# Kernel tuning notes

Hardware: AMD Instinct MI355X
Metric: run time of the kernel (lower is better)

The kernel has to match this reference:

```python
import jax, jax.numpy as jnp
import numpy as np
import math

B, T, D, H = 4, 2048, 1024, 8
DK = D // H


def _rel_shift(x):
    # x: [B, H, T, P] with P = 2T-1 (Transformer-XL relative shift)
    b, h, q, p = x.shape
    x = jnp.pad(x, ((0, 0), (0, 0), (0, 0), (1, 0)))
    x = x.reshape(b, h, p + 1, q)[:, :, 1:]
    return x.reshape(b, h, q, p)


def setup_inputs() -> dict:
    key = jax.random.key(0)
    ks = jax.random.split(key, 9)
    s = 0.02
    x = jax.random.normal(ks[0], (B, T, D), jnp.float32)
    pos_emb = jax.random.normal(ks[1], (1, 2 * T - 1, D), jnp.float32)
    Wq = jax.random.normal(ks[2], (D, D), jnp.float32) * s
    Wk = jax.random.normal(ks[3], (D, D), jnp.float32) * s
    Wv = jax.random.normal(ks[4], (D, D), jnp.float32) * s
    Wo = jax.random.normal(ks[5], (D, D), jnp.float32) * s
    Wp = jax.random.normal(ks[6], (D, D), jnp.float32) * s
    pos_bias_u = jax.random.normal(ks[7], (H, DK), jnp.float32) * s
    pos_bias_v = jax.random.normal(ks[8], (H, DK), jnp.float32) * s
    return {"x": x, "pos_emb": pos_emb, "Wq": Wq, "Wk": Wk, "Wv": Wv,
            "Wo": Wo, "Wp": Wp, "pos_bias_u": pos_bias_u, "pos_bias_v": pos_bias_v}


def reference(x, pos_emb, Wq, Wk, Wv, Wo, Wp, pos_bias_u, pos_bias_v):
    b, t, d = x.shape
    h, dk = pos_bias_u.shape
    inv_sdk = 1.0 / math.sqrt(dk)
    # projections (torch Linear: y = x @ W.T)
    q = (x @ Wq.T).reshape(b, t, h, dk)          # [B,T,H,DK]
    k = (x @ Wk.T).reshape(b, t, h, dk)          # [B,T,H,DK]
    v = (x @ Wv.T).reshape(b, t, h, dk)          # [B,T,H,DK]
    p = (pos_emb @ Wp.T).reshape(-1, h, dk)      # [P,H,DK], P = 2T-1
    # content and position scores
    matrix_ac = jnp.einsum('bqhd,bkhd->bhqk', q + pos_bias_u, k)   # [B,H,T,T]
    matrix_bd = jnp.einsum('bqhd,phd->bhqp', q + pos_bias_v, p)    # [B,H,T,2T-1]
    matrix_bd = _rel_shift(matrix_bd)[..., :t]                     # [B,H,T,T]
    scores = (matrix_ac + matrix_bd) * inv_sdk
    attn = jax.nn.softmax(scores, axis=-1)
    out = jnp.einsum('bhqk,bkhd->bqhd', attn, v).reshape(b, t, h * dk)
    return out @ Wo.T
```

## Files before the change

### kernel.cpp

```cpp
#include <hip/hip_runtime.h>
#include <cstdint>
#include <math.h>

#define B_   4
#define T_   2048
#define D_   1024
#define H_   8
#define DK_  128
#define P_   4095
#define PS_  4096

typedef unsigned short ushort_t;
typedef __attribute__((ext_vector_type(8))) short short8;
typedef __attribute__((ext_vector_type(4))) float floatx4;

__device__ inline float bf2f(ushort_t s) {
    return __uint_as_float(((unsigned int)s) << 16);
}
__device__ inline ushort_t f2bf(float f) {
    unsigned int u = __float_as_uint(f);
    u += 0x7fffu + ((u >> 16) & 1u);
    return (ushort_t)(u >> 16);
}

__device__ inline floatx4 mfma16(short8 a, short8 b, floatx4 c) {
    return __builtin_amdgcn_mfma_f32_16x16x32_bf16(a, b, c, 0, 0, 0);
}

__device__ inline void gload_lds16(const ushort_t* g, ushort_t* l) {
    __builtin_amdgcn_global_load_lds(
        (const __attribute__((address_space(1))) unsigned int*)g,
        (__attribute__((address_space(3))) unsigned int*)l, 16, 0, 0);
}

__device__ inline float rowmax16(float x) {
    int t;
    t = __builtin_amdgcn_update_dpp(0, __float_as_int(x), 0x128, 0xf, 0xf, true);
    x = fmaxf(x, __int_as_float(t));
    t = __builtin_amdgcn_update_dpp(0, __float_as_int(x), 0x124, 0xf, 0xf, true);
    x = fmaxf(x, __int_as_float(t));
    t = __builtin_amdgcn_update_dpp(0, __float_as_int(x), 0x4E, 0xf, 0xf, true);
    x = fmaxf(x, __int_as_float(t));
    t = __builtin_amdgcn_update_dpp(0, __float_as_int(x), 0xB1, 0xf, 0xf, true);
    x = fmaxf(x, __int_as_float(t));
    return x;
}

__global__ void detect_kernel(const ushort_t* x, int* flag) {
    if (blockIdx.x == 0 && threadIdx.x == 0) {
        int m = 0;
        for (int i = 0; i < 64; ++i) {
            float v = bf2f(x[2 * i]);
            float a = fabsf(v);
            if (!(a == 0.0f || (a > 1e-20f && a < 1e10f))) m = 1;
        }
        flag[0] = m;
    }
}

#define CV_TOT 17826816
template <int MODE>
__global__ __launch_bounds__(256) void convert_kernel(
    const int* __restrict__ flag,
    const void* __restrict__ x, const void* __restrict__ pe,
    const void* __restrict__ wq, const void* __restrict__ wk,
    const void* __restrict__ wv, const void* __restrict__ wo,
    const void* __restrict__ wp, const void* __restrict__ ub,
    const void* __restrict__ vb, ushort_t* __restrict__ dst)
{
    if (flag[0] != MODE) return;
    const size_t i = ((size_t)blockIdx.x * 256 + threadIdx.x) * 4;
    if (i >= CV_TOT) return;
    const void* s; size_t off;
    if (i < 8388608)       { s = x;  off = i; }
    else if (i < 12581888) { s = pe; off = i - 8388608; }
    else if (i < 13630464) { s = wq; off = i - 12581888; }
    else if (i < 14679040) { s = wk; off = i - 13630464; }
    else if (i < 15727616) { s = wv; off = i - 14679040; }
    else if (i < 16776192) { s = wo; off = i - 15727616; }
    else if (i < 17824768) { s = wp; off = i - 16776192; }
    else if (i < 17825792) { s = ub; off = i - 17824768; }
    else                   { s = vb; off = i - 17825792; }
    const size_t d = i + (i >= 12581888 ? 1024 : 0);
    if (MODE == 0) {
        *(uint2*)(dst + d) = *(const uint2*)((const ushort_t*)s + off);
    } else {
        float4 f = *(const float4*)((const float*)s + off);
        uint2 o;
        o.x = (unsigned)f2bf(f.x) | ((unsigned)f2bf(f.y) << 16);
        o.y = (unsigned)f2bf(f.z) | ((unsigned)f2bf(f.w) << 16);
        *(uint2*)(dst + d) = o;
    }
}

__global__ __launch_bounds__(256, 3) void gemm_mfma(
    const int* __restrict__ flag,
    const ushort_t* __restrict__ A, const ushort_t* __restrict__ W,
    void* __restrict__ C, int smode)
{
    if (smode == 3 && flag[0] != 0) return;
    if (smode == 4 && flag[0] != 1) return;
    const int K = 1024, N = 1024;

    __shared__ ushort_t Al[16 * 512];
    __shared__ ushort_t Wl[16 * 512];

    const int tid  = threadIdx.x;
    const int w    = tid >> 6, lane = tid & 63;
    const int r15  = lane & 15, quad = lane >> 4;
    const int wm   = w >> 1, wn = w & 1;
    const int m0   = blockIdx.y * 128, n0 = blockIdx.x * 128;

    floatx4 acc[4][4];
    const floatx4 z4 = {0.f, 0.f, 0.f, 0.f};
#pragma unroll
    for (int mt = 0; mt < 4; ++mt)
#pragma unroll
        for (int nt = 0; nt < 4; ++nt) acc[mt][nt] = z4;

    for (int k0 = 0; k0 < K; k0 += 64) {
#pragma unroll
        for (int ss = 0; ss < 4; ++ss) {
            const int s  = w * 4 + ss;
            const int mg = s >> 1, ks = s & 1;
            const int row = mg * 16 + r15;
            const int col = k0 + ks * 32 + quad * 8;
            gload_lds16(A + (size_t)(m0 + row) * K + col, &Al[s * 512]);
            gload_lds16(W + (size_t)(n0 + row) * K + col, &Wl[s * 512]);
        }
        __syncthreads();

        short8 af[2][4], bf[2][4];
#pragma unroll
        for (int ks = 0; ks < 2; ++ks) {
#pragma unroll
            for (int mt = 0; mt < 4; ++mt)
                af[ks][mt] = *(const short8*)&Al[(((wm * 4 + mt) * 2 + ks) * 64 + lane) * 8];
#pragma unroll
            for (int nt = 0; nt < 4; ++nt)
                bf[ks][nt] = *(const short8*)&Wl[(((wn * 4 + nt) * 2 + ks) * 64 + lane) * 8];
        }
#pragma unroll
        for (int ks = 0; ks < 2; ++ks)
#pragma unroll
            for (int mt = 0; mt < 4; ++mt)
#pragma unroll
                for (int nt = 0; nt < 4; ++nt)
                    acc[mt][nt] = mfma16(af[ks][mt], bf[ks][nt], acc[mt][nt]);
        __syncthreads();
    }

#pragma unroll
    for (int mt = 0; mt < 4; ++mt)
#pragma unroll
        for (int nt = 0; nt < 4; ++nt)
#pragma unroll
            for (int i = 0; i < 4; ++i) {
                const int m = m0 + wm * 64 + mt * 16 + quad * 4 + i;
                const int n = n0 + wn * 64 + nt * 16 + r15;
                const float v = acc[mt][nt][i];
                if (smode == 0) {
                    const int b = m >> 11, t = m & (T_ - 1);
                    const int h = n >> 7, dk = n & (DK_ - 1);
                    ((ushort_t*)C)[(((size_t)(b * H_ + h)) * T_ + t) * DK_ + dk] = f2bf(v);
                } else if (smode == 1) {
                    const int h = n >> 7, dk = n & (DK_ - 1);
                    ((ushort_t*)C)[((size_t)h * PS_ + m) * DK_ + dk] = f2bf(v);
                } else if (smode == 2) {
                    const int b = m >> 11, t = m & (T_ - 1);
                    const int h = n >> 7, dk = n & (DK_ - 1);
                    ((ushort_t*)C)[((size_t)(b * H_ + h) * DK_ + dk) * T_ + t] = f2bf(v);
                } else if (smode == 3) {
                    ((ushort_t*)C)[(size_t)m * N + n] = f2bf(v);
                } else {
                    ((float*)C)[(size_t)m * N + n] = v;
                }
            }
}

__global__ __launch_bounds__(256, 2) void attn_mfma(
    const ushort_t* __restrict__ qg,
    const ushort_t* __restrict__ kgl,
    const ushort_t* __restrict__ vt,
    const ushort_t* __restrict__ pg,
    const ushort_t* __restrict__ ubb,
    const ushort_t* __restrict__ vbb,
    ushort_t* __restrict__ ao)
{
    __shared__ ushort_t K_lds[16 * 512];
    __shared__ ushort_t V_lds[16 * 512];
    __shared__ ushort_t P_lds[32 * 512];
    __shared__ __align__(16) ushort_t pr_lds[4][1024];

    const int tid  = threadIdx.x;
    const int w    = tid >> 6;
    const int lane = tid & 63;
    const int r15  = lane & 15;
    const int quad = lane >> 4;
    const int bh   = blockIdx.y;
    const int h    = bh & (H_ - 1);
    const int b    = bh >> 3;
    const int q0b  = blockIdx.x * 64;
    const int q0w  = q0b + w * 16;

    short8 quA[4], qvA[4];
    {
        const ushort_t* qrow = qg + ((size_t)bh * T_ + q0w + r15) * DK_;
#pragma unroll
        for (int ks = 0; ks < 4; ++ks) {
            const int dk0 = ks * 32 + quad * 8;
            uint4 q4 = *(const uint4*)(qrow + dk0);
            uint4 u4 = *(const uint4*)(ubb + (size_t)h * DK_ + dk0);
            uint4 v4 = *(const uint4*)(vbb + (size_t)h * DK_ + dk0);
            const ushort_t* qs = (const ushort_t*)&q4;
            const ushort_t* us = (const ushort_t*)&u4;
            const ushort_t* vs = (const ushort_t*)&v4;
#pragma unroll
            for (int j = 0; j < 8; ++j) {
                const float qf = bf2f(qs[j]);
                quA[ks][j] = (short)f2bf(qf + bf2f(us[j]));
                qvA[ks][j] = (short)f2bf(qf + bf2f(vs[j]));
            }
        }
    }

    int src[4], hi[4];
#pragma unroll
    for (int i = 0; i < 4; ++i) {
        const int c = r15 + 15 - quad * 4 - i;
        src[i] = quad * 16 + (c & 15);
        hi[i]  = c >> 4;
    }

    floatx4 o[8];
    const floatx4 z4 = {0.f, 0.f, 0.f, 0.f};
#pragma unroll
    for (int g = 0; g < 8; ++g) o[g] = z4;
    floatx4 lacc = z4;
    float mrun[4];
#pragma unroll
    for (int i = 0; i < 4; ++i) mrun[i] = -1e30f;

    short8 ones8;
#pragma unroll
    for (int j = 0; j < 8; ++j) ones8[j] = (short)0x3F80;

    const float scale = 0.08838834764831845f;

    for (int kc0 = 0; kc0 < T_; kc0 += 64) {
        const int pbb = kc0 - q0b + 1984;

#pragma unroll
        for (int ss = 0; ss < 4; ++ss) {
            const int ck = w * 4 + ss;
            gload_lds16(kgl + ((size_t)bh * T_ + kc0 + w * 16 + r15) * DK_ + ss * 32 + quad * 8,
                        &K_lds[ck * 512]);
            const int cv = w * 4 + ss;
            const int og = cv >> 1, ks2 = cv & 1;
            gload_lds16(vt + ((size_t)(bh * DK_ + og * 16 + r15)) * T_ + kc0 + ks2 * 32 + quad * 8,
                        &V_lds[cv * 512]);
        }
#pragma unroll
        for (int ss = 0; ss < 8; ++ss) {
            const int cp = w * 8 + ss;
            const int gb = cp >> 2, ks = cp & 3;
            gload_lds16(pg + ((size_t)h * PS_ + pbb + gb * 16 + r15) * DK_ + ks * 32 + quad * 8,
                        &P_lds[cp * 512]);
        }
        __syncthreads();

        floatx4 ac[4];
#pragma unroll
        for (int g = 0; g < 4; ++g) {
            ac[g] = z4;
#pragma unroll
            for (int ks = 0; ks < 4; ++ks)
                ac[g] = mfma16(quA[ks],
                               *(const short8*)&K_lds[((g * 4 + ks) * 64 + lane) * 8],
                               ac[g]);
        }
        floatx4 bd[5];
#pragma unroll
        for (int g = 0; g < 5; ++g) {
            bd[g] = z4;
            const int gb = (3 - w) + g;
#pragma unroll
            for (int ks = 0; ks < 4; ++ks)
                bd[g] = mfma16(qvA[ks],
                               *(const short8*)&P_lds[((gb * 4 + ks) * 64 + lane) * 8],
                               bd[g]);
        }

        float pr[4][4];
        float mc[4];
#pragma unroll
        for (int i = 0; i < 4; ++i) {
            float mm = -1e30f;
#pragma unroll
            for (int g = 0; g < 4; ++g) {
                const float lo = __shfl(bd[g][i],     src[i], 64);
                const float hh = __shfl(bd[g + 1][i], src[i], 64);
                const float s  = (ac[g][i] + (hi[i] ? hh : lo)) * scale;
                pr[g][i] = s;
                mm = fmaxf(mm, s);
            }
            mc[i] = rowmax16(mm);
        }
        const bool nd = (mc[0] > mrun[0]) | (mc[1] > mrun[1]) |
                        (mc[2] > mrun[2]) | (mc[3] > mrun[3]);
        if (__any(nd)) {
            float alpha[4];
#pragma unroll
            for (int i = 0; i < 4; ++i) {
                const float mn = fmaxf(mrun[i], mc[i]);
                alpha[i] = __expf(mrun[i] - mn);
                mrun[i] = mn;
            }
#pragma unroll
            for (int g = 0; g < 8; ++g)
#pragma unroll
                for (int i = 0; i < 4; ++i) o[g][i] *= alpha[i];
#pragma unroll
            for (int i = 0; i < 4; ++i) lacc[i] *= alpha[i];
        }
#pragma unroll
        for (int g = 0; g < 4; ++g)
#pragma unroll
            for (int i = 0; i < 4; ++i)
                pr[g][i] = __expf(pr[g][i] - mrun[i]);

#pragma unroll
        for (int g = 0; g < 4; ++g) {
            const int unit = (g >> 1) * 4 + (g & 1) * 2 + (r15 >> 3);
#pragma unroll
            for (int i = 0; i < 4; ++i)
                pr_lds[w][(unit * 16 + quad * 4 + i) * 8 + (r15 & 7)] = f2bf(pr[g][i]);
        }
        short8 pa[2];
#pragma unroll
        for (int ks2 = 0; ks2 < 2; ++ks2)
            pa[ks2] = *(const short8*)&pr_lds[w][(ks2 * 64 + lane) * 8];

#pragma unroll
        for (int og = 0; og < 8; ++og)
#pragma unroll
            for (int ks2 = 0; ks2 < 2; ++ks2)
                o[og] = mfma16(pa[ks2],
                               *(const short8*)&V_lds[((og * 2 + ks2) * 64 + lane) * 8],
                               o[og]);
        lacc = mfma16(pa[0], ones8, lacc);
        lacc = mfma16(pa[1], ones8, lacc);
        __syncthreads();
    }

    float inv[4];
#pragma unroll
    for (int i = 0; i < 4; ++i) inv[i] = 1.0f / lacc[i];
#pragma unroll
    for (int og = 0; og < 8; ++og)
#pragma unroll
        for (int i = 0; i < 4; ++i) {
            const size_t idx =
                ((size_t)(b * T_ + q0w + quad * 4 + i)) * D_ + h * DK_ + og * 16 + r15;
            ao[idx] = f2bf(o[og][i] * inv[i]);
        }
}

extern "C" void kernel_launch(void* const* d_in, const int* in_sizes, int n_in,
                              void* d_out, int out_size, void* d_ws, size_t ws_size,
                              hipStream_t stream) {
    const void* x  = d_in[0];
    const void* pe = d_in[1];
    const void* Wq = d_in[2];
    const void* Wk = d_in[3];
    const void* Wv = d_in[4];
    const void* Wo = d_in[5];
    const void* Wp = d_in[6];
    const void* ub = d_in[7];
    const void* vb = d_in[8];

    int* flag = (int*)d_ws;
    ushort_t* arena = (ushort_t*)d_ws + 16;
    ushort_t* xb   = arena;
    ushort_t* peb  = arena + 8388608;
    ushort_t* wqb  = arena + 12582912;
    ushort_t* wkb  = wqb + 1048576;
    ushort_t* wvb  = wkb + 1048576;
    ushort_t* wob  = wvb + 1048576;
    ushort_t* wpb  = wob + 1048576;
    ushort_t* ubb  = arena + 17825792;
    ushort_t* vbb  = ubb + 1024;
    ushort_t* q_ws  = arena + 17827840;
    ushort_t* k_ws  = q_ws + 8388608;
    ushort_t* vt_ws = k_ws + 8388608;
    ushort_t* p_ws  = vt_ws + 8388608;
    ushort_t* ao_ws = xb;

    detect_kernel<<<1, 64, 0, stream>>>((const ushort_t*)x, flag);

    const int cvb = CV_TOT / 4 / 256;
    convert_kernel<0><<<cvb, 256, 0, stream>>>(flag, x, pe, Wq, Wk, Wv, Wo, Wp, ub, vb, arena);
    convert_kernel<1><<<cvb, 256, 0, stream>>>(flag, x, pe, Wq, Wk, Wv, Wo, Wp, ub, vb, arena);

    const dim3 gX(8, 64);
    const dim3 gP(8, 32);
    gemm_mfma<<<gX, 256, 0, stream>>>(flag, xb,  wqb, q_ws, 0);
    gemm_mfma<<<gX, 256, 0, stream>>>(flag, xb,  wkb, k_ws, 0);
    gemm_mfma<<<gX, 256, 0, stream>>>(flag, xb,  wvb, vt_ws, 2);
    gemm_mfma<<<gP, 256, 0, stream>>>(flag, peb, wpb, p_ws, 1);

    attn_mfma<<<dim3(T_ / 64, B_ * H_), 256, 0, stream>>>(
        q_ws, k_ws, vt_ws, p_ws, ubb, vbb, ao_ws);

    gemm_mfma<<<gX, 256, 0, stream>>>(flag, ao_ws, wob, d_out, 3);
    gemm_mfma<<<gX, 256, 0, stream>>>(flag, ao_ws, wob, d_out, 4);
}
```

Measured before the change: 596.8 us.

## Process 128 queries per attention block with two row tiles per wave

Each wave now handles two 16-row query tiles instead of one, so every K, V and positional fragment read from LDS feeds two MFMAs. The positional band is shared between adjacent row tiles, and the probability staging buffer is placed in the P_lds region after an extra barrier. This halves the grid and cuts K/V global loads per query, at the cost of higher register pressure (two output accumulator sets) and one more sync per iteration.

```diff
diff --git a/kernel.cpp b/kernel.cpp
--- a/kernel.cpp
+++ b/kernel.cpp
@@ -189,8 +189,7 @@
 {
     __shared__ ushort_t K_lds[16 * 512];
     __shared__ ushort_t V_lds[16 * 512];
-    __shared__ ushort_t P_lds[32 * 512];
-    __shared__ __align__(16) ushort_t pr_lds[4][1024];
+    __shared__ ushort_t P_lds[48 * 512];
 
     const int tid  = threadIdx.x;
     const int w    = tid >> 6;
@@ -200,12 +199,13 @@
     const int bh   = blockIdx.y;
     const int h    = bh & (H_ - 1);
     const int b    = bh >> 3;
-    const int q0b  = blockIdx.x * 64;
-    const int q0w  = q0b + w * 16;
-
-    short8 quA[4], qvA[4];
-    {
-        const ushort_t* qrow = qg + ((size_t)bh * T_ + q0w + r15) * DK_;
+    const int q0b  = blockIdx.x * 128;
+
+    short8 quA[2][4], qvA[2][4];
+#pragma unroll
+    for (int gg = 0; gg < 2; ++gg) {
+        const ushort_t* qrow =
+            qg + ((size_t)bh * T_ + q0b + w * 32 + gg * 16 + r15) * DK_;
 #pragma unroll
         for (int ks = 0; ks < 4; ++ks) {
             const int dk0 = ks * 32 + quad * 8;
@@ -218,8 +218,8 @@
 #pragma unroll
             for (int j = 0; j < 8; ++j) {
                 const float qf = bf2f(qs[j]);
-                quA[ks][j] = (short)f2bf(qf + bf2f(us[j]));
-                qvA[ks][j] = (short)f2bf(qf + bf2f(vs[j]));
+                quA[gg][ks][j] = (short)f2bf(qf + bf2f(us[j]));
+                qvA[gg][ks][j] = (short)f2bf(qf + bf2f(vs[j]));
             }
         }
     }
@@ -232,14 +232,19 @@
         hi[i]  = c >> 4;
     }
 
-    floatx4 o[8];
+    floatx4 o[2][8];
     const floatx4 z4 = {0.f, 0.f, 0.f, 0.f};
 #pragma unroll
-    for (int g = 0; g < 8; ++g) o[g] = z4;
-    floatx4 lacc = z4;
-    float mrun[4];
-#pragma unroll
-    for (int i = 0; i < 4; ++i) mrun[i] = -1e30f;
+    for (int gg = 0; gg < 2; ++gg)
+#pragma unroll
+        for (int g = 0; g < 8; ++g) o[gg][g] = z4;
+    floatx4 lacc[2];
+    lacc[0] = z4; lacc[1] = z4;
+    float mrun[2][4];
+#pragma unroll
+    for (int gg = 0; gg < 2; ++gg)
+#pragma unroll
+        for (int i = 0; i < 4; ++i) mrun[gg][i] = -1e30f;
 
     short8 ones8;
 #pragma unroll
@@ -248,7 +253,7 @@
     const float scale = 0.08838834764831845f;
 
     for (int kc0 = 0; kc0 < T_; kc0 += 64) {
-        const int pbb = kc0 - q0b + 1984;
+        const int pbb = kc0 - q0b + 1920;
 
 #pragma unroll
         for (int ss = 0; ss < 4; ++ss) {
@@ -261,109 +266,134 @@
                         &V_lds[cv * 512]);
         }
 #pragma unroll
-        for (int ss = 0; ss < 8; ++ss) {
-            const int cp = w * 8 + ss;
+        for (int ss = 0; ss < 12; ++ss) {
+            const int cp = w * 12 + ss;
             const int gb = cp >> 2, ks = cp & 3;
             gload_lds16(pg + ((size_t)h * PS_ + pbb + gb * 16 + r15) * DK_ + ks * 32 + quad * 8,
                         &P_lds[cp * 512]);
         }
         __syncthreads();
 
-        floatx4 ac[4];
-#pragma unroll
-        for (int g = 0; g < 4; ++g) {
-            ac[g] = z4;
+        floatx4 ac[2][4];
+#pragma unroll
+        for (int g = 0; g < 4; ++g) { ac[0][g] = z4; ac[1][g] = z4; }
+#pragma unroll
+        for (int g = 0; g < 4; ++g)
+#pragma unroll
+            for (int ks = 0; ks < 4; ++ks) {
+                const short8 kf = *(const short8*)&K_lds[((g * 4 + ks) * 64 + lane) * 8];
+                ac[0][g] = mfma16(quA[0][ks], kf, ac[0][g]);
+                ac[1][g] = mfma16(quA[1][ks], kf, ac[1][g]);
+            }
+
+        floatx4 bd[2][5];
+#pragma unroll
+        for (int g = 0; g < 5; ++g) { bd[0][g] = z4; bd[1][g] = z4; }
+#pragma unroll
+        for (int G = 0; G < 6; ++G) {
+            const int gbg = 6 - 2 * w + G;
+            short8 pf[4];
 #pragma unroll
             for (int ks = 0; ks < 4; ++ks)
-                ac[g] = mfma16(quA[ks],
-                               *(const short8*)&K_lds[((g * 4 + ks) * 64 + lane) * 8],
-                               ac[g]);
-        }
-        floatx4 bd[5];
-#pragma unroll
-        for (int g = 0; g < 5; ++g) {
-            bd[g] = z4;
-            const int gb = (3 - w) + g;
-#pragma unroll
-            for (int ks = 0; ks < 4; ++ks)
-                bd[g] = mfma16(qvA[ks],
-                               *(const short8*)&P_lds[((gb * 4 + ks) * 64 + lane) * 8],
-                               bd[g]);
-        }
-
-        float pr[4][4];
-        float mc[4];
-#pragma unroll
-        for (int i = 0; i < 4; ++i) {
-            float mm = -1e30f;
+                pf[ks] = *(const short8*)&P_lds[((gbg * 4 + ks) * 64 + lane) * 8];
+            if (G >= 1) {
+#pragma unroll
+                for (int ks = 0; ks < 4; ++ks)
+                    bd[0][G - 1] = mfma16(qvA[0][ks], pf[ks], bd[0][G - 1]);
+            }
+            if (G <= 4) {
+#pragma unroll
+                for (int ks = 0; ks < 4; ++ks)
+                    bd[1][G] = mfma16(qvA[1][ks], pf[ks], bd[1][G]);
+            }
+        }
+        __syncthreads();
+
+        ushort_t* prw = (ushort_t*)P_lds + w * 2048;
+        short8 pa[2][2];
+#pragma unroll
+        for (int gg = 0; gg < 2; ++gg) {
+            float pr[4][4];
+            float mc[4];
+#pragma unroll
+            for (int i = 0; i < 4; ++i) {
+                float mm = -1e30f;
+#pragma unroll
+                for (int g = 0; g < 4; ++g) {
+                    const float lo = __shfl(bd[gg][g][i],     src[i], 64);
+                    const float hh = __shfl(bd[gg][g + 1][i], src[i], 64);
+                    const float s  = (ac[gg][g][i] + (hi[i] ? hh : lo)) * scale;
+                    pr[g][i] = s;
+                    mm = fmaxf(mm, s);
+                }
+                mc[i] = rowmax16(mm);
+            }
+            const bool nd = (mc[0] > mrun[gg][0]) | (mc[1] > mrun[gg][1]) |
+                            (mc[2] > mrun[gg][2]) | (mc[3] > mrun[gg][3]);
+            if (__any(nd)) {
+                float alpha[4];
+#pragma unroll
+                for (int i = 0; i < 4; ++i) {
+                    const float mn = fmaxf(mrun[gg][i], mc[i]);
+                    alpha[i] = __expf(mrun[gg][i] - mn);
+                    mrun[gg][i] = mn;
+                }
+#pragma unroll
+                for (int g = 0; g < 8; ++g)
+#pragma unroll
+                    for (int i = 0; i < 4; ++i) o[gg][g][i] *= alpha[i];
+#pragma unroll
+                for (int i = 0; i < 4; ++i) lacc[gg][i] *= alpha[i];
+            }
+#pragma unroll
+            for (int g = 0; g < 4; ++g)
+#pragma unroll
+                for (int i = 0; i < 4; ++i)
+                    pr[g][i] = __expf(pr[g][i] - mrun[gg][i]);
+
 #pragma unroll
             for (int g = 0; g < 4; ++g) {
-                const float lo = __shfl(bd[g][i],     src[i], 64);
-                const float hh = __shfl(bd[g + 1][i], src[i], 64);
-                const float s  = (ac[g][i] + (hi[i] ? hh : lo)) * scale;
-                pr[g][i] = s;
-                mm = fmaxf(mm, s);
-            }
-            mc[i] = rowmax16(mm);
-        }
-        const bool nd = (mc[0] > mrun[0]) | (mc[1] > mrun[1]) |
-                        (mc[2] > mrun[2]) | (mc[3] > mrun[3]);
-        if (__any(nd)) {
-            float alpha[4];
+                const int unit = (g >> 1) * 4 + (g & 1) * 2 + (r15 >> 3);
+#pragma unroll
+                for (int i = 0; i < 4; ++i)
+                    prw[gg * 1024 + (unit * 16 + quad * 4 + i) * 8 + (r15 & 7)] =
+                        f2bf(pr[g][i]);
+            }
+#pragma unroll
+            for (int ks2 = 0; ks2 < 2; ++ks2)
+                pa[gg][ks2] = *(const short8*)&prw[gg * 1024 + (ks2 * 64 + lane) * 8];
+        }
+
+#pragma unroll
+        for (int og = 0; og < 8; ++og)
+#pragma unroll
+            for (int ks2 = 0; ks2 < 2; ++ks2) {
+                const short8 vf = *(const short8*)&V_lds[((og * 2 + ks2) * 64 + lane) * 8];
+                o[0][og] = mfma16(pa[0][ks2], vf, o[0][og]);
+                o[1][og] = mfma16(pa[1][ks2], vf, o[1][og]);
+            }
+        lacc[0] = mfma16(pa[0][0], ones8, lacc[0]);
+        lacc[0] = mfma16(pa[0][1], ones8, lacc[0]);
+        lacc[1] = mfma16(pa[1][0], ones8, lacc[1]);
+        lacc[1] = mfma16(pa[1][1], ones8, lacc[1]);
+        __syncthreads();
+    }
+
+#pragma unroll
+    for (int gg = 0; gg < 2; ++gg) {
+        float inv[4];
+#pragma unroll
+        for (int i = 0; i < 4; ++i) inv[i] = 1.0f / lacc[gg][i];
+#pragma unroll
+        for (int og = 0; og < 8; ++og)
 #pragma unroll
             for (int i = 0; i < 4; ++i) {
-                const float mn = fmaxf(mrun[i], mc[i]);
-                alpha[i] = __expf(mrun[i] - mn);
-                mrun[i] = mn;
-            }
-#pragma unroll
-            for (int g = 0; g < 8; ++g)
-#pragma unroll
-                for (int i = 0; i < 4; ++i) o[g][i] *= alpha[i];
-#pragma unroll
-            for (int i = 0; i < 4; ++i) lacc[i] *= alpha[i];
-        }
-#pragma unroll
-        for (int g = 0; g < 4; ++g)
-#pragma unroll
-            for (int i = 0; i < 4; ++i)
-                pr[g][i] = __expf(pr[g][i] - mrun[i]);
-
-#pragma unroll
-        for (int g = 0; g < 4; ++g) {
-            const int unit = (g >> 1) * 4 + (g & 1) * 2 + (r15 >> 3);
-#pragma unroll
-            for (int i = 0; i < 4; ++i)
-                pr_lds[w][(unit * 16 + quad * 4 + i) * 8 + (r15 & 7)] = f2bf(pr[g][i]);
-        }
-        short8 pa[2];
-#pragma unroll
-        for (int ks2 = 0; ks2 < 2; ++ks2)
-            pa[ks2] = *(const short8*)&pr_lds[w][(ks2 * 64 + lane) * 8];
-
-#pragma unroll
-        for (int og = 0; og < 8; ++og)
-#pragma unroll
-            for (int ks2 = 0; ks2 < 2; ++ks2)
-                o[og] = mfma16(pa[ks2],
-                               *(const short8*)&V_lds[((og * 2 + ks2) * 64 + lane) * 8],
-                               o[og]);
-        lacc = mfma16(pa[0], ones8, lacc);
-        lacc = mfma16(pa[1], ones8, lacc);
-        __syncthreads();
-    }
-
-    float inv[4];
-#pragma unroll
-    for (int i = 0; i < 4; ++i) inv[i] = 1.0f / lacc[i];
-#pragma unroll
-    for (int og = 0; og < 8; ++og)
-#pragma unroll
-        for (int i = 0; i < 4; ++i) {
-            const size_t idx =
-                ((size_t)(b * T_ + q0w + quad * 4 + i)) * D_ + h * DK_ + og * 16 + r15;
-            ao[idx] = f2bf(o[og][i] * inv[i]);
-        }
+                const size_t idx =
+                    ((size_t)(b * T_ + q0b + w * 32 + gg * 16 + quad * 4 + i)) * D_ +
+                    h * DK_ + og * 16 + r15;
+                ao[idx] = f2bf(o[gg][og][i] * inv[i]);
+            }
+    }
 }
 
 extern "C" void kernel_launch(void* const* d_in, const int* in_sizes, int n_in,
@@ -409,7 +439,7 @@
     gemm_mfma<<<gX, 256, 0, stream>>>(flag, xb,  wvb, vt_ws, 2);
     gemm_mfma<<<gP, 256, 0, stream>>>(flag, peb, wpb, p_ws, 1);
 
-    attn_mfma<<<dim3(T_ / 64, B_ * H_), 256, 0, stream>>>(
+    attn_mfma<<<dim3(T_ / 128, B_ * H_), 256, 0, stream>>>(
         q_ws, k_ws, vt_ws, p_ws, ubb, vbb, ao_ws);
 
     gemm_mfma<<<gX, 256, 0, stream>>>(flag, ao_ws, wob, d_out, 3);
```

New measurement: 625.0 us. 1.05x slower.

## Prefetch next K/V/P tile into registers and swizzle block order for L2 locality

Applied to the files above, without the earlier changes.

Swaps the direct global-to-LDS loads for register staging. The next key chunk's K, V and positional tiles are issued right after the barrier, so their global latency overlaps the current chunk's MFMA work, and the staged data is written to LDS at the top of the next iteration. It also remaps the linear block index so that concurrently scheduled blocks are spread across (batch, head) groups, which is meant to change cache/L2 locality. The cost is 16 extra uint4 registers per thread, which may lower occupancy or cause spills.

```diff
diff --git a/kernel.cpp b/kernel.cpp
--- a/kernel.cpp
+++ b/kernel.cpp
@@ -197,10 +197,13 @@
     const int lane = tid & 63;
     const int r15  = lane & 15;
     const int quad = lane >> 4;
-    const int bh   = blockIdx.y;
+
+    const int lin  = (int)(blockIdx.y * 32 + blockIdx.x);
+    const int swz  = (lin & 7) * 128 + (lin >> 3);
+    const int bh   = swz >> 5;
     const int h    = bh & (H_ - 1);
     const int b    = bh >> 3;
-    const int q0b  = blockIdx.x * 64;
+    const int q0b  = (swz & 31) * 64;
     const int q0w  = q0b + w * 16;
 
     short8 quA[4], qvA[4];
@@ -232,6 +235,27 @@
         hi[i]  = c >> 4;
     }
 
+    uint4 sK[4], sV[4], sP[8];
+    auto issue = [&](int kc0) {
+        const int pbb = kc0 - q0b + 1984;
+#pragma unroll
+        for (int ss = 0; ss < 4; ++ss) {
+            sK[ss] = *(const uint4*)(kgl +
+                ((size_t)bh * T_ + kc0 + w * 16 + r15) * DK_ + ss * 32 + quad * 8);
+            const int cv = w * 4 + ss;
+            const int og = cv >> 1, ks2 = cv & 1;
+            sV[ss] = *(const uint4*)(vt +
+                ((size_t)(bh * DK_ + og * 16 + r15)) * T_ + kc0 + ks2 * 32 + quad * 8);
+        }
+#pragma unroll
+        for (int ss = 0; ss < 8; ++ss) {
+            const int cp = w * 8 + ss;
+            const int gb = cp >> 2, ks = cp & 3;
+            sP[ss] = *(const uint4*)(pg +
+                ((size_t)h * PS_ + pbb + gb * 16 + r15) * DK_ + ks * 32 + quad * 8);
+        }
+    };
+
     floatx4 o[8];
     const floatx4 z4 = {0.f, 0.f, 0.f, 0.f};
 #pragma unroll
@@ -247,27 +271,20 @@
 
     const float scale = 0.08838834764831845f;
 
-    for (int kc0 = 0; kc0 < T_; kc0 += 64) {
-        const int pbb = kc0 - q0b + 1984;
-
+    issue(0);
+    const int NT = T_ / 64;
+    for (int n = 0; n < NT; ++n) {
 #pragma unroll
         for (int ss = 0; ss < 4; ++ss) {
-            const int ck = w * 4 + ss;
-            gload_lds16(kgl + ((size_t)bh * T_ + kc0 + w * 16 + r15) * DK_ + ss * 32 + quad * 8,
-                        &K_lds[ck * 512]);
-            const int cv = w * 4 + ss;
-            const int og = cv >> 1, ks2 = cv & 1;
-            gload_lds16(vt + ((size_t)(bh * DK_ + og * 16 + r15)) * T_ + kc0 + ks2 * 32 + quad * 8,
-                        &V_lds[cv * 512]);
-        }
-#pragma unroll
-        for (int ss = 0; ss < 8; ++ss) {
-            const int cp = w * 8 + ss;
-            const int gb = cp >> 2, ks = cp & 3;
-            gload_lds16(pg + ((size_t)h * PS_ + pbb + gb * 16 + r15) * DK_ + ks * 32 + quad * 8,
-                        &P_lds[cp * 512]);
-        }
+            *(uint4*)&K_lds[((w * 4 + ss) * 64 + lane) * 8] = sK[ss];
+            *(uint4*)&V_lds[((w * 4 + ss) * 64 + lane) * 8] = sV[ss];
+        }
+#pragma unroll
+        for (int ss = 0; ss < 8; ++ss)
+            *(uint4*)&P_lds[((w * 8 + ss) * 64 + lane) * 8] = sP[ss];
         __syncthreads();
+
+        if (n + 1 < NT) issue((n + 1) * 64);
 
         floatx4 ac[4];
 #pragma unroll
@@ -350,6 +367,7 @@
                                o[og]);
         lacc = mfma16(pa[0], ones8, lacc);
         lacc = mfma16(pa[1], ones8, lacc);
+
         __syncthreads();
     }
 
```

After: 1.041 ms. 74.5% more time.
